# Performance work log

Hardware: AMD Instinct MI355X
Metric: run time of the kernel (lower is better)

## Reference

```python
import jax, jax.numpy as jnp
import numpy as np

D_MODEL = 1024
H = 16
D_K = D_MODEL // H
D_FF = 4096
EPS = 1e-6


def setup_inputs() -> dict:
    key = jax.random.key(0)
    ks = jax.random.split(key, 16)
    s = 1.0 / np.sqrt(D_MODEL)
    sf = 1.0 / np.sqrt(D_FF)
    inp = {
        'x': jax.random.normal(ks[0], (4, 2048, D_MODEL), dtype=jnp.float32),
        'wq': jax.random.uniform(ks[1], (D_MODEL, D_MODEL), minval=-s, maxval=s),
        'bq': jax.random.uniform(ks[2], (D_MODEL,), minval=-s, maxval=s),
        'wk': jax.random.uniform(ks[3], (D_MODEL, D_MODEL), minval=-s, maxval=s),
        'bk': jax.random.uniform(ks[4], (D_MODEL,), minval=-s, maxval=s),
        'wv': jax.random.uniform(ks[5], (D_MODEL, D_MODEL), minval=-s, maxval=s),
        'bv': jax.random.uniform(ks[6], (D_MODEL,), minval=-s, maxval=s),
        'wo': jax.random.uniform(ks[7], (D_MODEL, D_MODEL), minval=-s, maxval=s),
        'bo': jax.random.uniform(ks[8], (D_MODEL,), minval=-s, maxval=s),
        'w1': jax.random.uniform(ks[9], (D_MODEL, D_FF), minval=-s, maxval=s),
        'b1': jax.random.uniform(ks[10], (D_FF,), minval=-s, maxval=s),
        'w2': jax.random.uniform(ks[11], (D_FF, D_MODEL), minval=-sf, maxval=sf),
        'b2': jax.random.uniform(ks[12], (D_MODEL,), minval=-sf, maxval=sf),
        'alpha1': jnp.ones((1,), jnp.float32),
        'bias1': jnp.zeros((1,), jnp.float32),
        'alpha2': jnp.ones((1,), jnp.float32),
        'bias2': jnp.zeros((1,), jnp.float32),
    }
    return inp


def _layer_norm(x, alpha, bias):
    # torch: alpha*(x-mean)/(std+eps)+bias with unbiased std (ddof=1), eps on std
    m = jnp.mean(x, axis=-1, keepdims=True)
    s = jnp.std(x, axis=-1, keepdims=True, ddof=1)
    return alpha * (x - m) / (s + EPS) + bias


def _mha(x, wq, bq, wk, bk, wv, bv, wo, bo):
    B, S, _ = x.shape
    q = (x @ wq + bq).reshape(B, S, H, D_K).transpose(0, 2, 1, 3)
    k = (x @ wk + bk).reshape(B, S, H, D_K).transpose(0, 2, 1, 3)
    v = (x @ wv + bv).reshape(B, S, H, D_K).transpose(0, 2, 1, 3)
    scores = jnp.einsum('bhqd,bhkd->bhqk', q, k) / np.sqrt(D_K)
    attn = jax.nn.softmax(scores, axis=-1)
    out = jnp.einsum('bhqk,bhkd->bhqd', attn, v)
    out = out.transpose(0, 2, 1, 3).reshape(B, S, D_MODEL)
    return out @ wo + bo


def reference(x, wq, bq, wk, bk, wv, bv, wo, bo, w1, b1, w2, b2,
              alpha1, bias1, alpha2, bias2):
    # Residual 1: x + MHA(LN(x))
    h = x + _mha(_layer_norm(x, alpha1, bias1), wq, bq, wk, bk, wv, bv, wo, bo)
    # Residual 2: h + FFN(LN(h)); FFN = W2 relu(W1 z + b1) + b2
    z = _layer_norm(h, alpha2, bias2)
    ffn = jax.nn.relu(z @ w1 + b1) @ w2 + b2
    return h + ffn
```

## Files before the change

kernel.cpp:

```cpp
#include <hip/hip_runtime.h>
#include <hip/hip_bf16.h>
#include <cstdint>
#include <cstddef>

typedef __bf16 bf16;
typedef __bf16 bf16x4 __attribute__((ext_vector_type(4)));
typedef __bf16 bf16x8 __attribute__((ext_vector_type(8)));
typedef float f32x4 __attribute__((ext_vector_type(4)));

#define AS1 __attribute__((address_space(1)))
#define AS3 __attribute__((address_space(3)))

__device__ __forceinline__ void gload_lds16(const void* g, void* l) {
  __builtin_amdgcn_global_load_lds((AS1 void*)g, (AS3 void*)l, 16, 0, 0);
}

__device__ __forceinline__ float b2f(unsigned short u) {
  union { unsigned int i; float f; } v; v.i = (unsigned int)u << 16; return v.f;
}

__global__ __launch_bounds__(256)
void transpose_cvt(const float* __restrict__ in, bf16* __restrict__ out,
                   int K, int N) {
  __shared__ float t[32][33];
  const int tx = threadIdx.x, ty = threadIdx.y;
  const int n0 = blockIdx.x * 32, k0 = blockIdx.y * 32;
#pragma unroll
  for (int j = ty; j < 32; j += 8)
    t[j][tx] = in[(size_t)(k0 + j) * N + n0 + tx];
  __syncthreads();
#pragma unroll
  for (int j = ty; j < 32; j += 8)
    out[(size_t)(n0 + j) * K + k0 + tx] = (bf16)t[tx][j];
}

__global__ __launch_bounds__(256)
void concat_bias(const float* __restrict__ bq, const float* __restrict__ bk,
                 const float* __restrict__ bv, float* __restrict__ o) {
  int i = blockIdx.x * 256 + threadIdx.x;
  if (i < 1024) o[i] = bq[i];
  else if (i < 2048) o[i] = bk[i - 1024];
  else o[i] = bv[i - 2048];
}

__global__ __launch_bounds__(256)
void ln_kernel(const float* __restrict__ x, bf16* __restrict__ y,
               const float* __restrict__ alpha_p, const float* __restrict__ beta_p) {
  const int row = blockIdx.x;
  const float4 v = ((const float4*)(x + (size_t)row * 1024))[threadIdx.x];
  float s = v.x + v.y + v.z + v.w;
  float ss = v.x * v.x + v.y * v.y + v.z * v.z + v.w * v.w;
#pragma unroll
  for (int m = 1; m < 64; m <<= 1) {
    s += __shfl_xor(s, m);
    ss += __shfl_xor(ss, m);
  }
  __shared__ float red[8];
  const int wave = threadIdx.x >> 6, lane = threadIdx.x & 63;
  if (lane == 0) { red[wave] = s; red[4 + wave] = ss; }
  __syncthreads();
  s = red[0] + red[1] + red[2] + red[3];
  ss = red[4] + red[5] + red[6] + red[7];
  const float mean = s * (1.0f / 1024.0f);
  const float var = fmaxf(ss - 1024.0f * mean * mean, 0.0f) * (1.0f / 1023.0f);
  const float k = alpha_p[0] / (sqrtf(var) + 1e-6f);
  const float beta = beta_p[0];
  union { bf16 b[4]; uint2 u; } pk;
  pk.b[0] = (bf16)((v.x - mean) * k + beta);
  pk.b[1] = (bf16)((v.y - mean) * k + beta);
  pk.b[2] = (bf16)((v.z - mean) * k + beta);
  pk.b[3] = (bf16)((v.w - mean) * k + beta);
  ((uint2*)(y + (size_t)row * 1024))[threadIdx.x] = pk.u;
}

template <typename OutT, bool RELU, bool RESID>
__global__ __launch_bounds__(256)
void gemm_bt(const bf16* __restrict__ A, const bf16* __restrict__ Bt,
             const float* __restrict__ bias, const float* __restrict__ resid,
             OutT* __restrict__ C, int M, int N, int K) {
  __shared__ __align__(16) bf16 As[2][128 * 32];
  __shared__ __align__(16) bf16 Bs[2][128 * 32];
  const int tid = threadIdx.x;
  const int wave = tid >> 6, lane = tid & 63;
  const int l16 = lane & 15, lq = lane >> 4;
  const int nwg = gridDim.x * gridDim.y;
  const int id = blockIdx.y * gridDim.x + blockIdx.x;
  const int w = (id & 7) * (nwg >> 3) + (id >> 3);
  const int bm = (w / gridDim.y) * 128, bn = (w % gridDim.y) * 128;
  const int wr = wave >> 1, wc = wave & 1;

  const int tmp = (lane * 16) ^ (((lane >> 3) & 7) << 4);
  const int srow = tmp >> 6, sseg = (tmp >> 4) & 3;
  const bf16* Ab = A + (size_t)bm * K + sseg * 8;
  const bf16* Bb = Bt + (size_t)bn * K + sseg * 8;

  auto STAGE = [&](int k0, int buf) {
#pragma unroll
    for (int i = 0; i < 2; i++) {
      const int chunk = wave * 2 + i;
      const int r = chunk * 16 + srow;
      gload_lds16(Ab + (size_t)r * K + k0, (char*)As[buf] + chunk * 1024);
      gload_lds16(Bb + (size_t)r * K + k0, (char*)Bs[buf] + chunk * 1024);
    }
  };
  auto swz = [&](int row) -> int {
    return (row >> 1) * 128 + (((((row & 1) << 2) | lq) ^ ((row >> 1) & 7)) << 4);
  };

  STAGE(0, 0);
  __syncthreads();

  f32x4 acc[4][4] = {};
  const int nk = K >> 5;
  for (int t = 0; t < nk; t++) {
    const int cur = t & 1;
    if (t + 1 < nk) STAGE((t + 1) << 5, cur ^ 1);
    bf16x8 a[4], b[4];
#pragma unroll
    for (int m = 0; m < 4; m++)
      a[m] = *(const bf16x8*)((const char*)As[cur] + swz(wr * 64 + m * 16 + l16));
#pragma unroll
    for (int n = 0; n < 4; n++)
      b[n] = *(const bf16x8*)((const char*)Bs[cur] + swz(wc * 64 + n * 16 + l16));
#pragma unroll
    for (int m = 0; m < 4; m++)
#pragma unroll
      for (int n = 0; n < 4; n++)
        acc[m][n] = __builtin_amdgcn_mfma_f32_16x16x32_bf16(a[m], b[n], acc[m][n], 0, 0, 0);
    __syncthreads();
  }
#pragma unroll
  for (int m = 0; m < 4; m++) {
    const int row0 = bm + wr * 64 + m * 16 + lq * 4;
#pragma unroll
    for (int n = 0; n < 4; n++) {
      const int col = bn + wc * 64 + n * 16 + l16;
      const float bv = bias[col];
#pragma unroll
      for (int j = 0; j < 4; j++) {
        float v = acc[m][n][j] + bv;
        if (RELU) v = fmaxf(v, 0.0f);
        if (RESID) v += resid[(size_t)(row0 + j) * N + col];
        C[(size_t)(row0 + j) * N + col] = (OutT)v;
      }
    }
  }
}

template <typename OutT, bool RELU, bool BIAS>
__global__ __launch_bounds__(512, 2)
void gemm_v4(const bf16* __restrict__ A, const bf16* __restrict__ Bt,
             const float* __restrict__ bias, OutT* __restrict__ C,
             int lda, int ldb, int ldc, int K,
             int azs, int bzs, size_t czs) {
  __shared__ __align__(16) char lds[3 * 32768];
  const int tid = threadIdx.x;
  const int wave = tid >> 6, lane = tid & 63;
  const int l16 = lane & 15, lq = lane >> 4;
  const int wr = wave >> 2, wc = wave & 3;
  const int nwg = gridDim.x * gridDim.y;
  const int id = blockIdx.y * gridDim.x + blockIdx.x;
  const int w = (id & 7) * (nwg >> 3) + (id >> 3);
  const int bm = (w / gridDim.y) * 256, bn = (w % gridDim.y) * 256;

  A  += (size_t)blockIdx.z * azs;
  Bt += (size_t)blockIdx.z * bzs;
  C  += (size_t)blockIdx.z * czs;

  const int p = lane >> 3, jj = (lane & 7) ^ p;
  const int lrow = p * 2 + (jj >> 2), lseg = jj & 3;
  const bf16* Abase = A + (size_t)bm * lda + lseg * 8;
  const bf16* Bbase = Bt + (size_t)bn * ldb + lseg * 8;

  auto STAGEQ = [&](int t, int qq) {
    const int k0 = t << 5;
    const int grow = (qq & 1) * 128 + wave * 16 + lrow;
    const void* src = (qq < 2) ? (const void*)(Abase + (size_t)grow * lda + k0)
                               : (const void*)(Bbase + (size_t)grow * ldb + k0);
    gload_lds16(src, lds + (t % 3) * 32768 + qq * 8192 + wave * 1024);
  };
  auto swz = [&](int row) -> int {
    return (row >> 1) * 128 + (((((row & 1) << 2) | lq) ^ ((row >> 1) & 7)) << 4);
  };

  const int nk = K >> 5;
#pragma unroll
  for (int qq = 0; qq < 4; qq++) STAGEQ(0, qq);
#pragma unroll
  for (int qq = 0; qq < 4; qq++) STAGEQ(1, qq);

  f32x4 acc[8][4] = {};
  for (int t = 0; t < nk; t++) {
    const char* buf = lds + (t % 3) * 32768;
    if (t + 1 < nk) asm volatile("s_waitcnt vmcnt(4)" ::: "memory");
    else            asm volatile("s_waitcnt vmcnt(0)" ::: "memory");
    __builtin_amdgcn_s_barrier();
    if (t + 2 < nk) { STAGEQ(t + 2, 0); STAGEQ(t + 2, 1); }
    bf16x8 a0[4], b0[4];
#pragma unroll
    for (int i = 0; i < 4; i++)
      a0[i] = *(const bf16x8*)(buf + swz(wr * 128 + i * 16 + l16));
#pragma unroll
    for (int n = 0; n < 4; n++)
      b0[n] = *(const bf16x8*)(buf + 16384 + swz(wc * 64 + n * 16 + l16));
    __builtin_amdgcn_s_barrier();
    asm volatile("s_waitcnt lgkmcnt(0)" ::: "memory");
    __builtin_amdgcn_sched_barrier(0);
    __builtin_amdgcn_s_setprio(1);
#pragma unroll
    for (int i = 0; i < 4; i++)
#pragma unroll
      for (int n = 0; n < 4; n++)
        acc[i][n] = __builtin_amdgcn_mfma_f32_16x16x32_bf16(a0[i], b0[n], acc[i][n], 0, 0, 0);
    __builtin_amdgcn_s_setprio(0);
    if (t + 2 < nk) { STAGEQ(t + 2, 2); STAGEQ(t + 2, 3); }
    bf16x8 a1[4];
#pragma unroll
    for (int i = 0; i < 4; i++)
      a1[i] = *(const bf16x8*)(buf + swz(wr * 128 + 64 + i * 16 + l16));
    __builtin_amdgcn_s_barrier();
    asm volatile("s_waitcnt lgkmcnt(0)" ::: "memory");
    __builtin_amdgcn_sched_barrier(0);
    __builtin_amdgcn_s_setprio(1);
#pragma unroll
    for (int i = 0; i < 4; i++)
#pragma unroll
      for (int n = 0; n < 4; n++)
        acc[4 + i][n] = __builtin_amdgcn_mfma_f32_16x16x32_bf16(a1[i], b0[n], acc[4 + i][n], 0, 0, 0);
    __builtin_amdgcn_s_setprio(0);
  }
#pragma unroll
  for (int m = 0; m < 8; m++) {
    const int row0 = bm + wr * 128 + m * 16 + lq * 4;
#pragma unroll
    for (int n = 0; n < 4; n++) {
      const int col = bn + wc * 64 + n * 16 + l16;
      const float bv = BIAS ? bias[col] : 0.0f;
#pragma unroll
      for (int j = 0; j < 4; j++) {
        float v = acc[m][n][j] + bv;
        if (RELU) v = fmaxf(v, 0.0f);
        C[(size_t)(row0 + j) * ldc + col] = (OutT)v;
      }
    }
  }
}

__global__ __launch_bounds__(256)
void ffn2_reduce(const bf16* __restrict__ p0, const bf16* __restrict__ p1,
                 const float* __restrict__ b2, float* __restrict__ out) {
  const size_t i = (size_t)blockIdx.x * 256 + threadIdx.x;
  float4 h = ((const float4*)out)[i];
  const ushort4 a = ((const ushort4*)p0)[i];
  const ushort4 b = ((const ushort4*)p1)[i];
  const float4 bb = ((const float4*)b2)[i & 255];
  h.x += b2f(a.x) + b2f(b.x) + bb.x;
  h.y += b2f(a.y) + b2f(b.y) + bb.y;
  h.z += b2f(a.z) + b2f(b.z) + bb.z;
  h.w += b2f(a.w) + b2f(b.w) + bb.w;
  ((float4*)out)[i] = h;
}

__global__ __launch_bounds__(256)
void vt_prep(const bf16* __restrict__ qkv, bf16* __restrict__ Vt) {
  __shared__ __align__(16) bf16 Vl[64 * 64];
  const int tid = threadIdx.x;
  const int sblk = blockIdx.x, bh = blockIdx.y, b = bh >> 4, h = bh & 15;
  const size_t srow = (size_t)b * 2048 + sblk * 64;
  const bf16* src = qkv + srow * 3072 + 2048 + h * 64;
#pragma unroll
  for (int i = 0; i < 2; i++) {
    int c = i * 256 + tid;
    int s = c >> 3, dseg = c & 7;
    int col = dseg ^ (s & 7) ^ (s >> 3);
    *(uint4*)((char*)Vl + s * 128 + col * 16) =
        *(const uint4*)(src + (size_t)s * 3072 + dseg * 8);
  }
  __syncthreads();
  bf16* dst = Vt + (size_t)bh * 64 * 2048 + sblk * 64;
#pragma unroll
  for (int i = 0; i < 2; i++) {
    int c = i * 256 + tid;
    int d = c >> 3, grp = c & 7;
    union { bf16 v[8]; uint4 u; } pk;
#pragma unroll
    for (int j = 0; j < 8; j++) {
      int s = grp * 8 + j;
      int col = (d >> 3) ^ (s & 7) ^ (s >> 3);
      pk.v[j] = *(const bf16*)((char*)Vl + s * 128 + col * 16 + ((2 * d) & 15));
    }
    *(uint4*)(dst + (size_t)d * 2048 + grp * 8) = pk.u;
  }
}

__global__ __launch_bounds__(256, 2)
void attn_kernel(const bf16* __restrict__ qkv, const bf16* __restrict__ Vt,
                 bf16* __restrict__ out) {
  __shared__ __align__(16) bf16 smem[32768];
  bf16* Qs = smem;
  bf16* Ks = smem + 16384;
  bf16* Vs = smem + 24576;
  const int tid = threadIdx.x, wave = tid >> 6, lane = tid & 63;
  const int l16 = lane & 15, lq = lane >> 4;
  const int id = blockIdx.y * 8 + blockIdx.x;
  const int w = (id & 7) * 64 + (id >> 3);
  const int qblk = w & 7, bh = w >> 3;
  const int b = bh >> 4, h = bh & 15;
  const int q0 = qblk * 256;
  const size_t rowbase = (size_t)b * 2048;
  const bf16* Qg = qkv + (rowbase + q0) * 3072 + h * 64;
  const bf16* Kg = qkv + rowbase * 3072 + 1024 + h * 64;
  const bf16* Vg = Vt + (size_t)bh * 64 * 2048;

#pragma unroll
  for (int i = 0; i < 8; i++) {
    const int c = i * 256 + wave * 64;
    const int cl = c + lane;
    const int r = cl >> 3, seg = cl & 7;
    gload_lds16(Qg + (size_t)r * 3072 + (seg ^ (r & 7)) * 8, (char*)Qs + c * 16);
  }
  auto stageKV = [&](int kt, int buf) {
    const int kv0 = kt * 64;
#pragma unroll
    for (int i = 0; i < 2; i++) {
      const int c = i * 256 + wave * 64;
      const int cl = c + lane;
      const int r = cl >> 3, seg = cl & 7;
      gload_lds16(Kg + (size_t)(kv0 + r) * 3072 + (seg ^ (r & 7)) * 8,
                  (char*)Ks + buf * 8192 + c * 16);
      gload_lds16(Vg + (size_t)r * 2048 + kv0 + (seg ^ (r & 7)) * 8,
                  (char*)Vs + buf * 8192 + c * 16);
    }
  };
  stageKV(0, 0);

  f32x4 oacc[4][4] = {};
  f32x4 lacc[4] = {};
  bf16x8 qb[4][2];
  bf16x8 onesb;
#pragma unroll
  for (int j = 0; j < 8; j++) onesb[j] = (bf16)1.0f;

  for (int t = 0; t < 32; t++) {
    const int cur = t & 1;
    __builtin_amdgcn_s_barrier();
    if (t < 31) stageKV(t + 1, cur ^ 1);
    if (t < 31) asm volatile("s_waitcnt vmcnt(4)" ::: "memory");
    else        asm volatile("s_waitcnt vmcnt(0)" ::: "memory");
    __builtin_amdgcn_s_barrier();
    const char* Kb = (const char*)Ks + cur * 8192;
    const char* Vb = (const char*)Vs + cur * 8192;

    if (t == 0) {
#pragma unroll
      for (int g = 0; g < 4; g++)
#pragma unroll
        for (int H = 0; H < 2; H++) {
          const int row = wave * 64 + g * 16 + l16;
          const int col = (H * 64 + lq * 16) ^ ((row & 7) << 4);
          qb[g][H] = *(const bf16x8*)((const char*)Qs + row * 128 + col);
        }
    }
    bf16x8 ka[2][4];
#pragma unroll
    for (int H = 0; H < 2; H++)
#pragma unroll
      for (int m = 0; m < 4; m++) {
        const int row = m * 16 + l16;
        const int col = (H * 64 + lq * 16) ^ ((row & 7) << 4);
        ka[H][m] = *(const bf16x8*)(Kb + row * 128 + col);
      }
    bf16x8 vb[2][4];
#pragma unroll
    for (int H = 0; H < 2; H++)
#pragma unroll
      for (int nd = 0; nd < 4; nd++) {
        const int row = nd * 16 + l16;
        const int xorv = (row & 7) << 4;
        const int c1 = (H * 64 + lq * 8) ^ xorv;
        const int c2 = (H * 64 + lq * 8 + 32) ^ xorv;
        bf16x4 lo = *(const bf16x4*)(Vb + row * 128 + c1);
        bf16x4 hi = *(const bf16x4*)(Vb + row * 128 + c2);
        vb[H][nd] = __builtin_shufflevector(lo, hi, 0, 1, 2, 3, 4, 5, 6, 7);
      }
#pragma unroll
    for (int g = 0; g < 4; g++) {
      f32x4 sc[4];
#pragma unroll
      for (int m = 0; m < 4; m++) {
        f32x4 z = {};
        sc[m] = __builtin_amdgcn_mfma_f32_16x16x32_bf16(ka[0][m], qb[g][0], z, 0, 0, 0);
        sc[m] = __builtin_amdgcn_mfma_f32_16x16x32_bf16(ka[1][m], qb[g][1], sc[m], 0, 0, 0);
      }
      bf16x8 pa0, pa1;
#pragma unroll
      for (int m = 0; m < 2; m++)
#pragma unroll
        for (int r = 0; r < 4; r++)
          pa0[m * 4 + r] = (bf16)__builtin_amdgcn_exp2f(sc[m][r] * 0.1803368801f);
#pragma unroll
      for (int m = 0; m < 2; m++)
#pragma unroll
        for (int r = 0; r < 4; r++)
          pa1[m * 4 + r] = (bf16)__builtin_amdgcn_exp2f(sc[2 + m][r] * 0.1803368801f);
#pragma unroll
      for (int nd = 0; nd < 4; nd++) {
        oacc[g][nd] = __builtin_amdgcn_mfma_f32_16x16x32_bf16(pa0, vb[0][nd], oacc[g][nd], 0, 0, 0);
        oacc[g][nd] = __builtin_amdgcn_mfma_f32_16x16x32_bf16(pa1, vb[1][nd], oacc[g][nd], 0, 0, 0);
      }
      lacc[g] = __builtin_amdgcn_mfma_f32_16x16x32_bf16(pa0, onesb, lacc[g], 0, 0, 0);
      lacc[g] = __builtin_amdgcn_mfma_f32_16x16x32_bf16(pa1, onesb, lacc[g], 0, 0, 0);
    }
  }
#pragma unroll
  for (int g = 0; g < 4; g++) {
#pragma unroll
    for (int r = 0; r < 4; r++) {
      const float inv = 1.0f / lacc[g][r];
      const size_t row = rowbase + q0 + wave * 64 + g * 16 + lq * 4 + r;
#pragma unroll
      for (int nd = 0; nd < 4; nd++)
        out[row * 1024 + h * 64 + nd * 16 + l16] = (bf16)(oacc[g][nd][r] * inv);
    }
  }
}

extern "C" void kernel_launch(void* const* d_in, const int* in_sizes, int n_in,
                              void* d_out, int out_size, void* d_ws, size_t ws_size,
                              hipStream_t stream) {
  const float* x      = (const float*)d_in[0];
  const float* wq     = (const float*)d_in[1];
  const float* bq     = (const float*)d_in[2];
  const float* wk     = (const float*)d_in[3];
  const float* bk     = (const float*)d_in[4];
  const float* wv     = (const float*)d_in[5];
  const float* bv     = (const float*)d_in[6];
  const float* wo     = (const float*)d_in[7];
  const float* bo     = (const float*)d_in[8];
  const float* w1     = (const float*)d_in[9];
  const float* b1     = (const float*)d_in[10];
  const float* w2     = (const float*)d_in[11];
  const float* b2     = (const float*)d_in[12];
  const float* alpha1 = (const float*)d_in[13];
  const float* bias1  = (const float*)d_in[14];
  const float* alpha2 = (const float*)d_in[15];
  const float* bias2  = (const float*)d_in[16];
  float* out = (float*)d_out;

  const size_t MB = 1024ull * 1024ull;
  char* ws = (char*)d_ws;
  bf16*  wqkvT = (bf16*)(ws);
  bf16*  woT   = (bf16*)(ws + 6 * MB);
  bf16*  w1T   = (bf16*)(ws + 8 * MB);
  bf16*  w2T   = (bf16*)(ws + 16 * MB);
  float* bqkv  = (float*)(ws + 24 * MB);
  bf16*  Z     = (bf16*)(ws + 24 * MB + 65536);
  bf16*  Vtb   = Z;
  bf16*  QKV   = (bf16*)(ws + 40 * MB + 65536);
  bf16*  AO    = (bf16*)(ws + 88 * MB + 65536);
  bf16*  FFN1  = QKV;
  bf16*  PART  = (bf16*)ws;
  const size_t PART1_OFF = (24 * MB + 65536) / 2;

  const dim3 tb(32, 8);
  transpose_cvt<<<dim3(32, 32), tb, 0, stream>>>(wq, wqkvT, 1024, 1024);
  transpose_cvt<<<dim3(32, 32), tb, 0, stream>>>(wk, wqkvT + 1024 * 1024, 1024, 1024);
  transpose_cvt<<<dim3(32, 32), tb, 0, stream>>>(wv, wqkvT + 2 * 1024 * 1024, 1024, 1024);
  transpose_cvt<<<dim3(32, 32), tb, 0, stream>>>(wo, woT, 1024, 1024);
  transpose_cvt<<<dim3(128, 32), tb, 0, stream>>>(w1, w1T, 1024, 4096);
  transpose_cvt<<<dim3(32, 128), tb, 0, stream>>>(w2, w2T, 4096, 1024);
  concat_bias<<<12, 256, 0, stream>>>(bq, bk, bv, bqkv);

  ln_kernel<<<8192, 256, 0, stream>>>(x, Z, alpha1, bias1);
  gemm_v4<bf16, false, true><<<dim3(32, 12), 512, 0, stream>>>(
      Z, wqkvT, bqkv, QKV, 1024, 1024, 3072, 1024, 0, 0, 0);
  vt_prep<<<dim3(32, 64), 256, 0, stream>>>(QKV, Vtb);
  attn_kernel<<<dim3(8, 64), 256, 0, stream>>>(QKV, Vtb, AO);
  gemm_bt<float, false, true><<<dim3(64, 8), 256, 0, stream>>>(
      AO, woT, bo, x, out, 8192, 1024, 1024);
  ln_kernel<<<8192, 256, 0, stream>>>(out, Z, alpha2, bias2);
  gemm_v4<bf16, true, true><<<dim3(32, 16), 512, 0, stream>>>(
      Z, w1T, b1, FFN1, 1024, 1024, 4096, 1024, 0, 0, 0);
  gemm_v4<bf16, false, false><<<dim3(32, 4, 2), 512, 0, stream>>>(
      FFN1, w2T, nullptr, PART, 4096, 4096, 1024, 2048, 2048, 2048, PART1_OFF);
  ffn2_reduce<<<8192, 256, 0, stream>>>(PART, PART + PART1_OFF, b2, out);
}
```

Before: 373.0 us.

## Triple-buffer attention KV, drop GEMM mid-loop barriers, permute V transpose layout

The GEMM main loop now issues both halves of the next-stage loads and all A/B fragment reads up front, and drops the two intra-iteration barriers and lgkmcnt waits, so the MFMAs rely on compiler-inserted waits. The attention kernel moves from double to triple buffering of K/V in LDS, prefetching two tiles ahead with one barrier per iteration. The V transpose writes keys in a permuted order so the attention kernel can read V fragments with a single 16-byte LDS load instead of two 8-byte loads. It also wraps MFMA phases in s_setprio. The costs are more LDS per attention block and reliance on the three-stage rotation alone to keep buffers from being overwritten while another wave still reads them.

```diff
diff --git a/kernel.cpp b/kernel.cpp
--- a/kernel.cpp
+++ b/kernel.cpp
@@ -195,16 +195,19 @@
     if (t + 1 < nk) asm volatile("s_waitcnt vmcnt(4)" ::: "memory");
     else            asm volatile("s_waitcnt vmcnt(0)" ::: "memory");
     __builtin_amdgcn_s_barrier();
+    __builtin_amdgcn_sched_barrier(0);
     if (t + 2 < nk) { STAGEQ(t + 2, 0); STAGEQ(t + 2, 1); }
-    bf16x8 a0[4], b0[4];
+    bf16x8 a0[4], b0[4], a1[4];
 #pragma unroll
     for (int i = 0; i < 4; i++)
       a0[i] = *(const bf16x8*)(buf + swz(wr * 128 + i * 16 + l16));
 #pragma unroll
     for (int n = 0; n < 4; n++)
       b0[n] = *(const bf16x8*)(buf + 16384 + swz(wc * 64 + n * 16 + l16));
-    __builtin_amdgcn_s_barrier();
-    asm volatile("s_waitcnt lgkmcnt(0)" ::: "memory");
+    if (t + 2 < nk) { STAGEQ(t + 2, 2); STAGEQ(t + 2, 3); }
+#pragma unroll
+    for (int i = 0; i < 4; i++)
+      a1[i] = *(const bf16x8*)(buf + swz(wr * 128 + 64 + i * 16 + l16));
     __builtin_amdgcn_sched_barrier(0);
     __builtin_amdgcn_s_setprio(1);
 #pragma unroll
@@ -213,13 +216,6 @@
       for (int n = 0; n < 4; n++)
         acc[i][n] = __builtin_amdgcn_mfma_f32_16x16x32_bf16(a0[i], b0[n], acc[i][n], 0, 0, 0);
     __builtin_amdgcn_s_setprio(0);
-    if (t + 2 < nk) { STAGEQ(t + 2, 2); STAGEQ(t + 2, 3); }
-    bf16x8 a1[4];
-#pragma unroll
-    for (int i = 0; i < 4; i++)
-      a1[i] = *(const bf16x8*)(buf + swz(wr * 128 + 64 + i * 16 + l16));
-    __builtin_amdgcn_s_barrier();
-    asm volatile("s_waitcnt lgkmcnt(0)" ::: "memory");
     __builtin_amdgcn_sched_barrier(0);
     __builtin_amdgcn_s_setprio(1);
 #pragma unroll
@@ -285,7 +281,8 @@
     union { bf16 v[8]; uint4 u; } pk;
 #pragma unroll
     for (int j = 0; j < 8; j++) {
-      int s = grp * 8 + j;
+      int pp = grp * 8 + j;
+      int s = (pp & 32) | (((pp >> 2) & 1) << 4) | (((pp >> 3) & 3) << 2) | (pp & 3);
       int col = (d >> 3) ^ (s & 7) ^ (s >> 3);
       pk.v[j] = *(const bf16*)((char*)Vl + s * 128 + col * 16 + ((2 * d) & 15));
     }
@@ -296,10 +293,10 @@
 __global__ __launch_bounds__(256, 2)
 void attn_kernel(const bf16* __restrict__ qkv, const bf16* __restrict__ Vt,
                  bf16* __restrict__ out) {
-  __shared__ __align__(16) bf16 smem[32768];
+  __shared__ __align__(16) bf16 smem[40960];
   bf16* Qs = smem;
   bf16* Ks = smem + 16384;
-  bf16* Vs = smem + 24576;
+  bf16* Vs = smem + 28672;
   const int tid = threadIdx.x, wave = tid >> 6, lane = tid & 63;
   const int l16 = lane & 15, lq = lane >> 4;
   const int id = blockIdx.y * 8 + blockIdx.x;
@@ -333,6 +330,7 @@
     }
   };
   stageKV(0, 0);
+  stageKV(1, 1);
 
   f32x4 oacc[4][4] = {};
   f32x4 lacc[4] = {};
@@ -342,14 +340,13 @@
   for (int j = 0; j < 8; j++) onesb[j] = (bf16)1.0f;
 
   for (int t = 0; t < 32; t++) {
-    const int cur = t & 1;
-    __builtin_amdgcn_s_barrier();
-    if (t < 31) stageKV(t + 1, cur ^ 1);
     if (t < 31) asm volatile("s_waitcnt vmcnt(4)" ::: "memory");
     else        asm volatile("s_waitcnt vmcnt(0)" ::: "memory");
     __builtin_amdgcn_s_barrier();
-    const char* Kb = (const char*)Ks + cur * 8192;
-    const char* Vb = (const char*)Vs + cur * 8192;
+    __builtin_amdgcn_sched_barrier(0);
+    if (t + 2 < 32) stageKV(t + 2, (t + 2) % 3);
+    const char* Kb = (const char*)Ks + (t % 3) * 8192;
+    const char* Vb = (const char*)Vs + (t % 3) * 8192;
 
     if (t == 0) {
 #pragma unroll
@@ -376,22 +373,20 @@
 #pragma unroll
       for (int nd = 0; nd < 4; nd++) {
         const int row = nd * 16 + l16;
-        const int xorv = (row & 7) << 4;
-        const int c1 = (H * 64 + lq * 8) ^ xorv;
-        const int c2 = (H * 64 + lq * 8 + 32) ^ xorv;
-        bf16x4 lo = *(const bf16x4*)(Vb + row * 128 + c1);
-        bf16x4 hi = *(const bf16x4*)(Vb + row * 128 + c2);
-        vb[H][nd] = __builtin_shufflevector(lo, hi, 0, 1, 2, 3, 4, 5, 6, 7);
+        const int col = (H * 64 + lq * 16) ^ ((row & 7) << 4);
+        vb[H][nd] = *(const bf16x8*)(Vb + row * 128 + col);
       }
 #pragma unroll
     for (int g = 0; g < 4; g++) {
       f32x4 sc[4];
+      __builtin_amdgcn_s_setprio(1);
 #pragma unroll
       for (int m = 0; m < 4; m++) {
         f32x4 z = {};
         sc[m] = __builtin_amdgcn_mfma_f32_16x16x32_bf16(ka[0][m], qb[g][0], z, 0, 0, 0);
         sc[m] = __builtin_amdgcn_mfma_f32_16x16x32_bf16(ka[1][m], qb[g][1], sc[m], 0, 0, 0);
       }
+      __builtin_amdgcn_s_setprio(0);
       bf16x8 pa0, pa1;
 #pragma unroll
       for (int m = 0; m < 2; m++)
@@ -403,6 +398,7 @@
 #pragma unroll
         for (int r = 0; r < 4; r++)
           pa1[m * 4 + r] = (bf16)__builtin_amdgcn_exp2f(sc[2 + m][r] * 0.1803368801f);
+      __builtin_amdgcn_s_setprio(1);
 #pragma unroll
       for (int nd = 0; nd < 4; nd++) {
         oacc[g][nd] = __builtin_amdgcn_mfma_f32_16x16x32_bf16(pa0, vb[0][nd], oacc[g][nd], 0, 0, 0);
@@ -410,6 +406,7 @@
       }
       lacc[g] = __builtin_amdgcn_mfma_f32_16x16x32_bf16(pa0, onesb, lacc[g], 0, 0, 0);
       lacc[g] = __builtin_amdgcn_mfma_f32_16x16x32_bf16(pa1, onesb, lacc[g], 0, 0, 0);
+      __builtin_amdgcn_s_setprio(0);
     }
   }
 #pragma unroll
```

After: 370.6 us. Within noise of the previous version (-0.7%).
